# Performance work log

Measured on AMD Instinct MI355X. Metric: run time of the kernel, lower is better.

Reference implementation:

```python
import jax, jax.numpy as jnp
import numpy as np


def _centers(n):
    # make_coord_3d: cell-center coordinates in (-1, 1)
    r = 1.0 / n
    return -1.0 + r + 2.0 * r * jnp.arange(n, dtype=jnp.float32)


def setup_inputs() -> dict:
    key = jax.random.key(0)
    ks = jax.random.split(key, 16)
    B, C, Tin, Hin, Win = 1, 64, 6, 40, 40
    Gc = 27 + 8 * C  # 539 channels into conv00_3d
    s = lambda k, shp: jax.random.normal(k, shp, dtype=jnp.float32) * 0.05
    return {
        "feat": jax.random.normal(ks[0], (B, C, Tin, Hin, Win), dtype=jnp.float32),
        # conv00_3d = depthwise(1x1x1, groups=Gc) + pointwise(Gc->256)
        "dw1_w": s(ks[1], (Gc,)), "dw1_b": s(ks[2], (Gc,)),
        "pw1_w": s(ks[3], (256, Gc)), "pw1_b": s(ks[4], (256,)),
        "fc1_w": s(ks[5], (256, 256)), "fc1_b": s(ks[6], (256,)),
        "fc2_w": s(ks[7], (3, 256)), "fc2_b": s(ks[8], (3,)),
        # short_cut = depthwise(1x1x1, groups=C) + pointwise(C->3)
        "sc_dw_w": s(ks[9], (C,)), "sc_dw_b": s(ks[10], (C,)),
        "sc_pw_w": s(ks[11], (3, C)), "sc_pw_b": s(ks[12], (3,)),
        "T_out": 12, "H_out": 80, "W_out": 80,
    }


def _pw(x, w, b):
    # 1x1x1 Conv3d
    return jnp.einsum('bcthw,oc->bothw', x, w) + b[None, :, None, None, None]


def _forward(feat, dw1_w, dw1_b, pw1_w, pw1_b, fc1_w, fc1_b, fc2_w, fc2_b,
             sc_dw_w, sc_dw_b, sc_pw_w, sc_pw_b, T_out, H_out, W_out):
    B, C, Tin, Hin, Win = feat.shape
    ct, ch, cw = _centers(T_out), _centers(H_out), _centers(W_out)  # target centers
    lt, lh, lw = _centers(Tin), _centers(Hin), _centers(Win)        # low-res centers
    rt, rx, ry = 1.0 / Tin, 1.0 / Hin, 1.0 / Win                    # 2/N/2 radii
    eps = 1e-6

    def near(c, n):
        # grid_sample nearest, align_corners=False; coords pre-clamped as in torch code
        cc = jnp.clip(c, -1.0 + 1e-6, 1.0 - 1e-6)
        return jnp.clip(jnp.round(((cc + 1.0) * n - 1.0) / 2.0), 0, n - 1).astype(jnp.int32)

    rel_coords, feat_s, areas = [], [], []
    for vt in (-1.0, 1.0):
        for vx in (-1.0, 1.0):
            for vy in (-1.0, 1.0):
                it = near(ct + vt * rt + eps, Tin)   # [T'] (separable per-dim)
                ih = near(ch + vx * rx + eps, Hin)   # [H']
                iw = near(cw + vy * ry + eps, Win)   # [W']
                f = feat[:, :, it[:, None, None], ih[None, :, None], iw[None, None, :]]
                dct = (ct - lt[it]) * Tin
                dch = (ch - lh[ih]) * Hin
                dcw = (cw - lw[iw]) * Win
                rel = jnp.stack([
                    jnp.broadcast_to(dct[:, None, None], (T_out, H_out, W_out)),
                    jnp.broadcast_to(dch[None, :, None], (T_out, H_out, W_out)),
                    jnp.broadcast_to(dcw[None, None, :], (T_out, H_out, W_out)),
                ], axis=0)
                rel = jnp.broadcast_to(rel[None], (B, 3, T_out, H_out, W_out))
                area = (jnp.abs(dct)[:, None, None] * jnp.abs(dch)[None, :, None]
                        * jnp.abs(dcw)[None, None, :]) + 1e-9
                rel_coords.append(rel)
                feat_s.append(f)
                areas.append(area)

    tot = sum(areas)
    areas_sw = areas[::-1]  # pairwise swaps 0<->7, 1<->6, 2<->5, 3<->4
    feat_s = [f * (a / tot)[None, None] for f, a in zip(feat_s, areas_sw)]

    # rel_cell: (2/size * scale) * in_size == 2.0 on every axis
    rel_cell = jnp.full((B, 3, T_out, H_out, W_out), 2.0, dtype=feat.dtype)

    grid = jnp.concatenate([*rel_coords, *feat_s, rel_cell], axis=1)  # [B,27+8C,T',H',W']

    x = _pw(grid * dw1_w[None, :, None, None, None] + dw1_b[None, :, None, None, None],
            pw1_w, pw1_b)
    ret = _pw(jax.nn.gelu(_pw(x, fc1_w, fc1_b), approximate=False), fc2_w, fc2_b)

    # short cut: depthwise-separable 1x1x1 conv, then trilinear grid_sample (border pad)
    sc = _pw(feat * sc_dw_w[None, :, None, None, None] + sc_dw_b[None, :, None, None, None],
             sc_pw_w, sc_pw_b)

    def lin_idx(c, n):
        x = jnp.clip(((c + 1.0) * n - 1.0) / 2.0, 0.0, n - 1.0)  # border padding: clip coord
        x0 = jnp.floor(x)
        frac = x - x0
        i0 = x0.astype(jnp.int32)
        i1 = jnp.minimum(i0 + 1, n - 1)
        return i0, i1, frac

    t0, t1, ft = lin_idx(ct, Tin)
    h0, h1, fh = lin_idx(ch, Hin)
    w0, w1, fw = lin_idx(cw, Win)
    g = sc[:, :, t0] * (1 - ft)[None, None, :, None, None] + sc[:, :, t1] * ft[None, None, :, None, None]
    g = g[:, :, :, h0] * (1 - fh)[None, None, None, :, None] + g[:, :, :, h1] * fh[None, None, None, :, None]
    g = g[:, :, :, :, w0] * (1 - fw) + g[:, :, :, :, w1] * fw
    return ret + g


def reference(feat, dw1_w, dw1_b, pw1_w, pw1_b, fc1_w, fc1_b, fc2_w, fc2_b,
              sc_dw_w, sc_dw_b, sc_pw_w, sc_pw_b, T_out, H_out, W_out):
    return _forward(feat, dw1_w, dw1_b, pw1_w, pw1_b, fc1_w, fc1_b, fc2_w, fc2_b,
                    sc_dw_w, sc_dw_b, sc_pw_w, sc_pw_b, T_out, H_out, W_out)
```

## Files before the change

kernel.cpp:

```cpp
#include <hip/hip_runtime.h>
#include <hip/hip_bf16.h>

using bf16 = __hip_bfloat16;
typedef __attribute__((ext_vector_type(8))) short short8x;
typedef __attribute__((ext_vector_type(4))) short short4x;
typedef __attribute__((ext_vector_type(4))) unsigned short ushort4x;
typedef __attribute__((ext_vector_type(4))) float f32x4;

__device__ __forceinline__ float b2f(bf16 x) { return __bfloat162float(x); }
__device__ __forceinline__ bf16  f2b(float x) { return __float2bfloat16(x); }
__device__ __forceinline__ short bbits(float x) { bf16 b = f2b(x); short s; __builtin_memcpy(&s, &b, 2); return s; }
__device__ __forceinline__ float bu2f(unsigned short s) {
    unsigned v = ((unsigned)s) << 16; float f; __builtin_memcpy(&f, &v, 4); return f;
}
__device__ __forceinline__ float ldin(const void* p, int i, int f32) {
    return f32 ? ((const float*)p)[i] : b2f(((const bf16*)p)[i]);
}

#define TI 6
#define HI 40
#define WI 40
#define TO 12
#define HO 80
#define WO 80
#define NIN (TI*HI*WI)
#define NOUT (TO*HO*WO)

#define F_B1    0
#define F_ACO   (F_B1 + 256)
#define F_SCW   (F_ACO + 6*256)
#define F_SCB   (F_SCW + 3*64)
#define F_SC    (F_SCB + 4)
#define F_DT    (F_SC + 3*NIN)
#define F_DH    (F_DT + 2*TO)
#define F_DW    (F_DH + 2*HO)
#define F_FT    (F_DW + 2*WO)
#define F_FH    (F_FT + TO)
#define F_FW    (F_FH + HO)
#define F_FC1B  (F_FW + WO)
#define F_FC2W  (F_FC1B + 256)
#define F_FC2B  (F_FC2W + 768)
#define F_END   (F_FC2B + 4)
#define I_IT    0
#define I_IH    (I_IT + 2*TO)
#define I_IW    (I_IH + 2*HO)
#define I_LT0   (I_IW + 2*WO)
#define I_LT1   (I_LT0 + TO)
#define I_LH0   (I_LT1 + TO)
#define I_LH1   (I_LH0 + HO)
#define I_LW0   (I_LH1 + HO)
#define I_LW1   (I_LW0 + WO)
#define I_FLAG  (I_LW1 + WO)
#define I_END   (I_FLAG + 1)

#define MPOS 32
#define ZPAD 264
#define FT_S 72

__device__ __forceinline__ void axis_tables(int i, int n_out, int n_in,
                                            float* dvals, int* ivals,
                                            int* l0, int* l1, float* fr) {
    const float r_out = 1.0f / (float)n_out;
    const float r_in  = 1.0f / (float)n_in;
    const float c = -1.0f + r_out + 2.0f * r_out * (float)i;
    #pragma unroll
    for (int v = 0; v < 2; ++v) {
        const float vv = v ? 1.0f : -1.0f;
        float cc = c + vv * r_in + 1e-6f;
        cc = fminf(fmaxf(cc, -1.0f + 1e-6f), 1.0f - 1e-6f);
        float fx = rintf(((cc + 1.0f) * (float)n_in - 1.0f) * 0.5f);
        fx = fminf(fmaxf(fx, 0.0f), (float)(n_in - 1));
        const int idx = (int)fx;
        const float l = -1.0f + r_in + 2.0f * r_in * (float)idx;
        dvals[v * n_out + i] = (c - l) * (float)n_in;
        ivals[v * n_out + i] = idx;
    }
    float x = fminf(fmaxf(((c + 1.0f) * (float)n_in - 1.0f) * 0.5f, 0.0f), (float)(n_in - 1));
    const float x0 = floorf(x);
    fr[i] = x - x0;
    const int i0 = (int)x0;
    l0[i] = i0;
    l1[i] = min(i0 + 1, n_in - 1);
}

__global__ __launch_bounds__(256)
void k_setup(const void* __restrict__ feat,
             const void* __restrict__ dw1_w, const void* __restrict__ dw1_b,
             const void* __restrict__ pw1_w, const void* __restrict__ pw1_b,
             const void* __restrict__ fc1_w, const void* __restrict__ fc1_b,
             const void* __restrict__ fc2_w, const void* __restrict__ fc2_b,
             const void* __restrict__ sc_dw_w, const void* __restrict__ sc_dw_b,
             const void* __restrict__ sc_pw_w, const void* __restrict__ sc_pw_b,
             bf16* __restrict__ fc1P, bf16* __restrict__ W1fP,
             float* __restrict__ F, int* __restrict__ I) {
    const int tid = threadIdx.x;
    const int b = blockIdx.x;
    __shared__ int sflag;
    if (tid < 64) {
        const unsigned short* u = (const unsigned short*)feat;
        const unsigned e = (u[2 * tid] >> 7) & 0xFFu;
        const unsigned long long m = __ballot(e >= 0x68u && e <= 0x8Eu);
        if (tid == 0) sflag = (__popcll(m) < 32) ? 1 : 0;
    }
    __syncthreads();
    const int f32 = sflag;

    if (b >= 288) {
        const int g = (b - 288) * 256 + tid;
        const int k = g >> 11, kc = (g >> 10) & 1, nt = (g >> 6) & 15, wl = g & 63;
        const int n = nt * 16 + (wl & 15);
        const int k0 = kc * 32 + (wl >> 4) * 8;
        bf16 v[8];
        #pragma unroll
        for (int jj = 0; jj < 8; ++jj) {
            const int ch = 24 + k * 64 + k0 + jj;
            v[jj] = f2b(ldin(pw1_w, n * 539 + ch, f32) * ldin(dw1_w, ch, f32));
        }
        *(short8x*)&W1fP[(size_t)g * 8] = *(short8x*)v;
        return;
    }
    if (b >= 256) {
        const int g = (b - 256) * 256 + tid;
        const int kc = g >> 10, nt = (g >> 6) & 15, wl = g & 63;
        const int n = nt * 16 + (wl & 15);
        const int k0 = kc * 32 + (wl >> 4) * 8;
        bf16 v[8];
        #pragma unroll
        for (int jj = 0; jj < 8; ++jj) v[jj] = f2b(ldin(fc1_w, n * 256 + k0 + jj, f32));
        *(short8x*)&fc1P[(size_t)g * 8] = *(short8x*)v;
        return;
    }

    __shared__ float row[539];
    __shared__ float red[256];
    const int o = b;

    for (int ch = tid; ch < 539; ch += 256) row[ch] = ldin(pw1_w, o * 539 + ch, f32);
    __syncthreads();

    float s = 0.f;
    for (int ch = tid; ch < 539; ch += 256) s += row[ch] * ldin(dw1_b, ch, f32);
    red[tid] = s;
    __syncthreads();
    for (int st = 128; st > 0; st >>= 1) {
        if (tid < st) red[tid] += red[tid + st];
        __syncthreads();
    }

    if (tid == 0) {
        float bacc = ldin(pw1_b, o, f32) + red[0];
        #pragma unroll
        for (int ch = 536; ch < 539; ++ch)
            bacc += 2.0f * row[ch] * ldin(dw1_w, ch, f32);
        F[F_B1 + o] = bacc;

        float A[6] = {0.f, 0.f, 0.f, 0.f, 0.f, 0.f};
        #pragma unroll
        for (int k = 0; k < 8; ++k) {
            A[(k >> 2)]           += row[3*k + 0] * ldin(dw1_w, 3*k + 0, f32);
            A[2 + ((k >> 1) & 1)] += row[3*k + 1] * ldin(dw1_w, 3*k + 1, f32);
            A[4 + (k & 1)]        += row[3*k + 2] * ldin(dw1_w, 3*k + 2, f32);
        }
        #pragma unroll
        for (int i = 0; i < 6; ++i) F[F_ACO + i * 256 + o] = A[i];
    }

    if (b == 0) {
        if (tid == 0) I[I_FLAG] = f32;
        F[F_FC1B + tid] = ldin(fc1_b, tid, f32);
        for (int r = tid; r < 768; r += 256) F[F_FC2W + r] = ldin(fc2_w, r, f32);
        if (tid < 3) F[F_FC2B + tid] = ldin(fc2_b, tid, f32);
        if (tid < 3) {
            const int j = tid;
            float sb = ldin(sc_pw_b, j, f32);
            for (int c = 0; c < 64; ++c) {
                const float pw = ldin(sc_pw_w, j * 64 + c, f32);
                F[F_SCW + j * 64 + c] = pw * ldin(sc_dw_w, c, f32);
                sb += pw * ldin(sc_dw_b, c, f32);
            }
            F[F_SCB + j] = sb;
        }
        if (tid < TO) axis_tables(tid, TO, TI, F + F_DT, I + I_IT, I + I_LT0, I + I_LT1, F + F_FT);
        if (tid < HO) axis_tables(tid, HO, HI, F + F_DH, I + I_IH, I + I_LH0, I + I_LH1, F + F_FH);
        if (tid < WO) axis_tables(tid, WO, WI, F + F_DW, I + I_IW, I + I_LW0, I + I_LW1, F + F_FW);
    }
}

__global__ __launch_bounds__(256)
void k_corner(const void* __restrict__ feat, float* __restrict__ F,
              const int* __restrict__ I, const bf16* __restrict__ W1fP,
              bf16* __restrict__ P) {
    const int tid = threadIdx.x;
    const int pt = blockIdx.x, k = blockIdx.y;
    const int pos0 = pt * 32;
    const int f32 = I[I_FLAG];

    __shared__ __align__(16) short ft[32 * FT_S];
    __shared__ __align__(16) short zt[32 * ZPAD];

    {
        const int p = tid & 31, c0 = tid >> 5;
        #pragma unroll
        for (int cc = 0; cc < 8; ++cc) {
            const int c = c0 * 8 + cc;
            ft[p * FT_S + c] = bbits(ldin(feat, c * NIN + pos0 + p, f32));
        }
    }
    __syncthreads();

    const int wl = tid & 63, w = tid >> 6;
    const int col = wl & 15, quad = wl >> 4;
    f32x4 acc[2][4] = { { {0,0,0,0},{0,0,0,0},{0,0,0,0},{0,0,0,0} },
                        { {0,0,0,0},{0,0,0,0},{0,0,0,0},{0,0,0,0} } };
    const short8x* bp = (const short8x*)W1fP;
    #pragma unroll
    for (int kc = 0; kc < 2; ++kc) {
        const short8x a0 = *(const short8x*)&ft[col * FT_S + kc * 32 + quad * 8];
        const short8x a1 = *(const short8x*)&ft[(col + 16) * FT_S + kc * 32 + quad * 8];
        #pragma unroll
        for (int nt = 0; nt < 4; ++nt) {
            const short8x bb = bp[((k * 2 + kc) * 16 + (w * 4 + nt)) * 64 + wl];
            acc[0][nt] = __builtin_amdgcn_mfma_f32_16x16x32_bf16(a0, bb, acc[0][nt], 0, 0, 0);
            acc[1][nt] = __builtin_amdgcn_mfma_f32_16x16x32_bf16(a1, bb, acc[1][nt], 0, 0, 0);
        }
    }

    if (k == 0 && tid < 96) {
        const int j = tid >> 5, p = tid & 31;
        float s = F[F_SCB + j];
        for (int c = 0; c < 64; ++c)
            s += bu2f((unsigned short)ft[p * FT_S + c]) * F[F_SCW + j * 64 + c];
        F[F_SC + j * NIN + pos0 + p] = s;
    }

    #pragma unroll
    for (int mt = 0; mt < 2; ++mt)
        #pragma unroll
        for (int nt = 0; nt < 4; ++nt) {
            const int n = w * 64 + nt * 16 + col;
            #pragma unroll
            for (int r = 0; r < 4; ++r)
                zt[(mt * 16 + quad * 4 + r) * ZPAD + n] = bbits(acc[mt][nt][r]);
        }
    __syncthreads();

    #pragma unroll
    for (int q = 0; q < 4; ++q) {
        const int i = q * 256 + tid;
        const int p = i >> 5, c8 = i & 31;
        const short8x v = *(const short8x*)&zt[p * ZPAD + c8 * 8];
        *(short8x*)(P + ((size_t)(k * NIN + pos0 + p)) * 256 + c8 * 8) = v;
    }
}

__global__ __launch_bounds__(256, 4)
void k_main(const bf16* __restrict__ P, const bf16* __restrict__ fc1P,
            const float* __restrict__ F, const int* __restrict__ I,
            void* __restrict__ outv) {
    const int tid = threadIdx.x;
    const int pos0 = blockIdx.x * MPOS;
    const int f32 = I[I_FLAG];

    __shared__ __align__(16) short zsh[MPOS * ZPAD];
    __shared__ float redc[MPOS * 4 * 3];
    __shared__ int   sh_ipos[MPOS][8];
    __shared__ float sh_wk[MPOS][8];
    __shared__ float sh_dv[MPOS][6];
    __shared__ float sh_g[3][MPOS];

    if (tid < MPOS) {
        const int p = tid;
        const int pos = pos0 + p;
        const int t = pos / (HO * WO);
        const int rem = pos - t * (HO * WO);
        const int h = rem / WO;
        const int w = rem - h * WO;
        const int   iTa[2] = { I[I_IT + t], I[I_IT + TO + t] };
        const float dTv[2] = { F[F_DT + t], F[F_DT + TO + t] };
        const int   iHa[2] = { I[I_IH + h], I[I_IH + HO + h] };
        const float dHv[2] = { F[F_DH + h], F[F_DH + HO + h] };
        const int   iWa[2] = { I[I_IW + w], I[I_IW + WO + w] };
        const float dWv[2] = { F[F_DW + w], F[F_DW + WO + w] };
        sh_dv[p][0] = dTv[0]; sh_dv[p][1] = dTv[1];
        sh_dv[p][2] = dHv[0]; sh_dv[p][3] = dHv[1];
        sh_dv[p][4] = dWv[0]; sh_dv[p][5] = dWv[1];
        const float aT[2] = { fabsf(dTv[0]), fabsf(dTv[1]) };
        const float aH[2] = { fabsf(dHv[0]), fabsf(dHv[1]) };
        const float aW[2] = { fabsf(dWv[0]), fabsf(dWv[1]) };
        const float tot = (aT[0] + aT[1]) * (aH[0] + aH[1]) * (aW[0] + aW[1]) + 8e-9f;
        #pragma unroll
        for (int k = 0; k < 8; ++k) {
            const int at = k >> 2, ah = (k >> 1) & 1, aw = k & 1;
            sh_wk[p][k] = (aT[1 - at] * aH[1 - ah] * aW[1 - aw] + 1e-9f) / tot;
            sh_ipos[p][k] = iTa[at] * (HI * WI) + iHa[ah] * WI + iWa[aw];
        }
        const int a0 = I[I_LT0 + t], a1 = I[I_LT1 + t];
        const int bh0 = I[I_LH0 + h], bh1 = I[I_LH1 + h];
        const int c0 = I[I_LW0 + w], c1 = I[I_LW1 + w];
        const float fT = F[F_FT + t], fH = F[F_FH + h], fW = F[F_FW + w];
        #pragma unroll
        for (int jj = 0; jj < 3; ++jj) {
            const float* Sj = F + F_SC + jj * NIN;
            const int i0 = a0 * (HI * WI), i1 = a1 * (HI * WI);
            const float v000 = Sj[i0 + bh0 * WI + c0], v001 = Sj[i0 + bh0 * WI + c1];
            const float v010 = Sj[i0 + bh1 * WI + c0], v011 = Sj[i0 + bh1 * WI + c1];
            const float v100 = Sj[i1 + bh0 * WI + c0], v101 = Sj[i1 + bh0 * WI + c1];
            const float v110 = Sj[i1 + bh1 * WI + c0], v111 = Sj[i1 + bh1 * WI + c1];
            const float u00 = v000 * (1.f - fT) + v100 * fT;
            const float u01 = v001 * (1.f - fT) + v101 * fT;
            const float u10 = v010 * (1.f - fT) + v110 * fT;
            const float u11 = v011 * (1.f - fT) + v111 * fT;
            const float q0 = u00 * (1.f - fH) + u10 * fH;
            const float q1 = u01 * (1.f - fH) + u11 * fH;
            sh_g[jj][p] = q0 * (1.f - fW) + q1 * fW;
        }
    }
    __syncthreads();

    {
        const int og = tid & 63, pg = tid >> 6;
        const int o4 = og * 4;
        const float4 bz = *(const float4*)&F[F_B1 + o4];
        float4 Ac[6];
        #pragma unroll
        for (int i = 0; i < 6; ++i) Ac[i] = *(const float4*)&F[F_ACO + i * 256 + o4];
        for (int pp = 0; pp < 8; ++pp) {
            const int p = pg * 8 + pp;
            float a0 = bz.x, a1 = bz.y, a2 = bz.z, a3 = bz.w;
            #pragma unroll
            for (int i = 0; i < 6; ++i) {
                const float dv = sh_dv[p][i];
                a0 += Ac[i].x * dv; a1 += Ac[i].y * dv;
                a2 += Ac[i].z * dv; a3 += Ac[i].w * dv;
            }
            #pragma unroll
            for (int k = 0; k < 8; ++k) {
                const float wk = sh_wk[p][k];
                const ushort4x u = *(const ushort4x*)(P + ((size_t)(k * NIN + sh_ipos[p][k]) * 256 + o4));
                a0 += wk * bu2f(u.x); a1 += wk * bu2f(u.y);
                a2 += wk * bu2f(u.z); a3 += wk * bu2f(u.w);
            }
            short4x zz = { bbits(a0), bbits(a1), bbits(a2), bbits(a3) };
            *(short4x*)&zsh[p * ZPAD + o4] = zz;
        }
    }
    __syncthreads();

    {
        const int wl = tid & 63, w = tid >> 6;
        const int col = wl & 15, quad = wl >> 4;
        f32x4 acc0[4] = { {0,0,0,0}, {0,0,0,0}, {0,0,0,0}, {0,0,0,0} };
        f32x4 acc1[4] = { {0,0,0,0}, {0,0,0,0}, {0,0,0,0}, {0,0,0,0} };
        const short8x* bp = (const short8x*)fc1P;
        #pragma unroll
        for (int kc = 0; kc < 8; ++kc) {
            const short8x a0 = *(const short8x*)&zsh[col * ZPAD + kc * 32 + quad * 8];
            const short8x a1 = *(const short8x*)&zsh[(col + 16) * ZPAD + kc * 32 + quad * 8];
            #pragma unroll
            for (int nt = 0; nt < 4; ++nt) {
                const short8x b = bp[(kc * 16 + w * 4 + nt) * 64 + wl];
                acc0[nt] = __builtin_amdgcn_mfma_f32_16x16x32_bf16(a0, b, acc0[nt], 0, 0, 0);
                acc1[nt] = __builtin_amdgcn_mfma_f32_16x16x32_bf16(a1, b, acc1[nt], 0, 0, 0);
            }
        }
        float part[2][3][4];
        #pragma unroll
        for (int mt = 0; mt < 2; ++mt)
            #pragma unroll
            for (int jj = 0; jj < 3; ++jj)
                #pragma unroll
                for (int r = 0; r < 4; ++r) part[mt][jj][r] = 0.f;
        #pragma unroll
        for (int nt = 0; nt < 4; ++nt) {
            const int j = w * 64 + nt * 16 + col;
            const float fb = F[F_FC1B + j];
            const float w0 = F[F_FC2W + j];
            const float w1 = F[F_FC2W + 256 + j];
            const float w2 = F[F_FC2W + 512 + j];
            #pragma unroll
            for (int r = 0; r < 4; ++r) {
                float x = acc0[nt][r] + fb;
                float hh = 0.5f * x * (1.0f + erff(x * 0.70710678118654752f));
                part[0][0][r] += w0 * hh; part[0][1][r] += w1 * hh; part[0][2][r] += w2 * hh;
                x = acc1[nt][r] + fb;
                hh = 0.5f * x * (1.0f + erff(x * 0.70710678118654752f));
                part[1][0][r] += w0 * hh; part[1][1][r] += w1 * hh; part[1][2][r] += w2 * hh;
            }
        }
        #pragma unroll
        for (int m = 1; m <= 8; m <<= 1)
            #pragma unroll
            for (int mt = 0; mt < 2; ++mt)
                #pragma unroll
                for (int jj = 0; jj < 3; ++jj)
                    #pragma unroll
                    for (int r = 0; r < 4; ++r)
                        part[mt][jj][r] += __shfl_xor(part[mt][jj][r], m, 64);
        if (col == 0) {
            #pragma unroll
            for (int mt = 0; mt < 2; ++mt)
                #pragma unroll
                for (int jj = 0; jj < 3; ++jj)
                    #pragma unroll
                    for (int r = 0; r < 4; ++r) {
                        const int p = mt * 16 + quad * 4 + r;
                        redc[(p * 4 + w) * 3 + jj] = part[mt][jj][r];
                    }
        }
    }
    __syncthreads();

    if (tid < 96) {
        const int p = tid / 3, jj = tid - 3 * p;
        float a = F[F_FC2B + jj] + sh_g[jj][p];
        #pragma unroll
        for (int w = 0; w < 4; ++w) a += redc[(p * 4 + w) * 3 + jj];
        const int oidx = jj * NOUT + pos0 + p;
        if (f32) ((float*)outv)[oidx] = a;
        else     ((bf16*)outv)[oidx] = f2b(a);
    }
}

extern "C" void kernel_launch(void* const* d_in, const int* in_sizes, int n_in,
                              void* d_out, int out_size, void* d_ws, size_t ws_size,
                              hipStream_t stream) {
    const void* feat    = d_in[0];
    const void* dw1_w   = d_in[1];
    const void* dw1_b   = d_in[2];
    const void* pw1_w   = d_in[3];
    const void* pw1_b   = d_in[4];
    const void* fc1_w   = d_in[5];
    const void* fc1_b   = d_in[6];
    const void* fc2_w   = d_in[7];
    const void* fc2_b   = d_in[8];
    const void* sc_dw_w = d_in[9];
    const void* sc_dw_b = d_in[10];
    const void* sc_pw_w = d_in[11];
    const void* sc_pw_b = d_in[12];

    const size_t P_BYTES    = (size_t)8 * NIN * 256 * 2;
    const size_t FC1P_BYTES = (size_t)256 * 256 * 2;
    const size_t W1FP_BYTES = (size_t)8 * 64 * 256 * 2;
    bf16*  P    = (bf16*)d_ws;
    bf16*  fc1P = (bf16*)((char*)d_ws + P_BYTES);
    bf16*  W1fP = (bf16*)((char*)d_ws + P_BYTES + FC1P_BYTES);
    float* F    = (float*)((char*)d_ws + P_BYTES + FC1P_BYTES + W1FP_BYTES);
    int*   I    = (int*)(F + F_END);

    k_setup<<<352, 256, 0, stream>>>(feat, dw1_w, dw1_b, pw1_w, pw1_b, fc1_w, fc1_b,
                                     fc2_w, fc2_b, sc_dw_w, sc_dw_b, sc_pw_w, sc_pw_b,
                                     fc1P, W1fP, F, I);
    k_corner<<<dim3(NIN / 32, 8), 256, 0, stream>>>(feat, F, I, W1fP, P);
    k_main<<<NOUT / MPOS, 256, 0, stream>>>(P, fc1P, F, I, (void*)d_out);
}
```

Before: 171.7 us.

## Fold per-corner projection into main kernel via weighted gather plus MFMA

Removes the k_corner kernel that precomputed a 256-channel projection for every input voxel and each of 8 corners (a large bf16 intermediate). The main kernel now gathers the weighted 64-channel transposed features for each of the 8 corners into shared memory and runs a K=512 MFMA against the folded pw1 weights. Setup is restructured to write a transposed bf16 feature buffer and compute the shortcut conv, and erf in GELU is replaced by a polynomial approximation. This cuts memory traffic and one launch, but adds more MFMA work per output and slightly changes rounding, since weights are applied before the bf16 cast and GELU is approximated.

Measured after the change: 199.1 us. 1.16x slower.

```diff
diff --git a/kernel.cpp b/kernel.cpp
--- a/kernel.cpp
+++ b/kernel.cpp
@@ -3,8 +3,6 @@
 
 using bf16 = __hip_bfloat16;
 typedef __attribute__((ext_vector_type(8))) short short8x;
-typedef __attribute__((ext_vector_type(4))) short short4x;
-typedef __attribute__((ext_vector_type(4))) unsigned short ushort4x;
 typedef __attribute__((ext_vector_type(4))) float f32x4;
 
 __device__ __forceinline__ float b2f(bf16 x) { return __bfloat162float(x); }
@@ -15,6 +13,15 @@
 }
 __device__ __forceinline__ float ldin(const void* p, int i, int f32) {
     return f32 ? ((const float*)p)[i] : b2f(((const bf16*)p)[i]);
+}
+
+__device__ __forceinline__ float gelu_f(float x) {
+    const float z = fabsf(x) * 0.70710678118654752f;
+    const float t = __builtin_amdgcn_rcpf(1.0f + 0.3275911f * z);
+    const float poly = t * (0.254829592f + t * (-0.284496736f +
+                       t * (1.421413741f + t * (-1.453152027f + t * 1.061405429f))));
+    const float erfv = 1.0f - poly * __expf(-z * z);
+    return 0.5f * x * (1.0f + copysignf(erfv, x));
 }
 
 #define TI 6
@@ -28,9 +35,7 @@
 
 #define F_B1    0
 #define F_ACO   (F_B1 + 256)
-#define F_SCW   (F_ACO + 6*256)
-#define F_SCB   (F_SCW + 3*64)
-#define F_SC    (F_SCB + 4)
+#define F_SC    (F_ACO + 6*256)
 #define F_DT    (F_SC + 3*NIN)
 #define F_DH    (F_DT + 2*TO)
 #define F_DW    (F_DH + 2*HO)
@@ -54,8 +59,9 @@
 #define I_END   (I_FLAG + 1)
 
 #define MPOS 32
+#define USTR 552
+#define CSTR 68
 #define ZPAD 264
-#define FT_S 72
 
 __device__ __forceinline__ void axis_tables(int i, int n_out, int n_in,
                                             float* dvals, int* ivals,
@@ -91,8 +97,8 @@
              const void* __restrict__ fc2_w, const void* __restrict__ fc2_b,
              const void* __restrict__ sc_dw_w, const void* __restrict__ sc_dw_b,
              const void* __restrict__ sc_pw_w, const void* __restrict__ sc_pw_b,
-             bf16* __restrict__ fc1P, bf16* __restrict__ W1fP,
-             float* __restrict__ F, int* __restrict__ I) {
+             bf16* __restrict__ featT, bf16* __restrict__ fc1P,
+             bf16* __restrict__ W1fP, float* __restrict__ F, int* __restrict__ I) {
     const int tid = threadIdx.x;
     const int b = blockIdx.x;
     __shared__ int sflag;
@@ -105,163 +111,130 @@
     __syncthreads();
     const int f32 = sflag;
 
-    if (b >= 288) {
-        const int g = (b - 288) * 256 + tid;
-        const int k = g >> 11, kc = (g >> 10) & 1, nt = (g >> 6) & 15, wl = g & 63;
-        const int n = nt * 16 + (wl & 15);
-        const int k0 = kc * 32 + (wl >> 4) * 8;
-        bf16 v[8];
-        #pragma unroll
-        for (int jj = 0; jj < 8; ++jj) {
-            const int ch = 24 + k * 64 + k0 + jj;
-            v[jj] = f2b(ldin(pw1_w, n * 539 + ch, f32) * ldin(dw1_w, ch, f32));
-        }
-        *(short8x*)&W1fP[(size_t)g * 8] = *(short8x*)v;
+    if (b < 16) {
+        const int nt = b;
+        __shared__ float rowb[16][540];
+        __shared__ float dwl[544];
+        __shared__ float dbl[544];
+        for (int ch = tid; ch < 539; ch += 256) {
+            dwl[ch] = ldin(dw1_w, ch, f32);
+            dbl[ch] = ldin(dw1_b, ch, f32);
+        }
+        for (int r = 0; r < 16; ++r)
+            for (int ch = tid; ch < 539; ch += 256)
+                rowb[r][ch] = ldin(pw1_w, (nt * 16 + r) * 539 + ch, f32);
+        __syncthreads();
+
+        {
+            const int r = tid >> 4, part = tid & 15;
+            float s = 0.f;
+            for (int ch = part; ch < 539; ch += 16) s += rowb[r][ch] * dbl[ch];
+            #pragma unroll
+            for (int m = 1; m <= 8; m <<= 1) s += __shfl_xor(s, m, 64);
+            if (part == 0) {
+                const int n = nt * 16 + r;
+                float bacc = ldin(pw1_b, n, f32) + s;
+                #pragma unroll
+                for (int ch = 536; ch < 539; ++ch) bacc += 2.0f * rowb[r][ch] * dwl[ch];
+                F[F_B1 + n] = bacc;
+                float A[6] = {0.f, 0.f, 0.f, 0.f, 0.f, 0.f};
+                #pragma unroll
+                for (int k = 0; k < 8; ++k) {
+                    A[(k >> 2)]           += rowb[r][3*k + 0] * dwl[3*k + 0];
+                    A[2 + ((k >> 1) & 1)] += rowb[r][3*k + 1] * dwl[3*k + 1];
+                    A[4 + (k & 1)]        += rowb[r][3*k + 2] * dwl[3*k + 2];
+                }
+                #pragma unroll
+                for (int i = 0; i < 6; ++i) F[F_ACO + i * 256 + n] = A[i];
+            }
+        }
+        for (int it = 0; it < 4; ++it) {
+            const int gl = it * 256 + tid;
+            const int kc = gl >> 6, wl = gl & 63;
+            const int nl = wl & 15;
+            const int K0 = kc * 32 + (wl >> 4) * 8;
+            bf16 v[8];
+            #pragma unroll
+            for (int jj = 0; jj < 8; ++jj)
+                v[jj] = f2b(rowb[nl][24 + K0 + jj] * dwl[24 + K0 + jj]);
+            *(short8x*)&W1fP[((size_t)(kc * 16 + nt) * 64 + wl) * 8] = *(short8x*)v;
+        }
         return;
     }
-    if (b >= 256) {
-        const int g = (b - 256) * 256 + tid;
-        const int kc = g >> 10, nt = (g >> 6) & 15, wl = g & 63;
-        const int n = nt * 16 + (wl & 15);
-        const int k0 = kc * 32 + (wl >> 4) * 8;
-        bf16 v[8];
-        #pragma unroll
-        for (int jj = 0; jj < 8; ++jj) v[jj] = f2b(ldin(fc1_w, n * 256 + k0 + jj, f32));
-        *(short8x*)&fc1P[(size_t)g * 8] = *(short8x*)v;
+    if (b < 32) {
+        const int nt = b - 16;
+        __shared__ float rowf[16][260];
+        for (int r = 0; r < 16; ++r)
+            rowf[r][tid] = ldin(fc1_w, (nt * 16 + r) * 256 + tid, f32);
+        __syncthreads();
+        for (int it = 0; it < 2; ++it) {
+            const int gl = it * 256 + tid;
+            const int kc = gl >> 6, wl = gl & 63;
+            const int nl = wl & 15;
+            const int K0 = kc * 32 + (wl >> 4) * 8;
+            bf16 v[8];
+            #pragma unroll
+            for (int jj = 0; jj < 8; ++jj) v[jj] = f2b(rowf[nl][K0 + jj]);
+            *(short8x*)&fc1P[((size_t)(kc * 16 + nt) * 64 + wl) * 8] = *(short8x*)v;
+        }
         return;
     }
-
-    __shared__ float row[539];
-    __shared__ float red[256];
-    const int o = b;
-
-    for (int ch = tid; ch < 539; ch += 256) row[ch] = ldin(pw1_w, o * 539 + ch, f32);
-    __syncthreads();
-
-    float s = 0.f;
-    for (int ch = tid; ch < 539; ch += 256) s += row[ch] * ldin(dw1_b, ch, f32);
-    red[tid] = s;
-    __syncthreads();
-    for (int st = 128; st > 0; st >>= 1) {
-        if (tid < st) red[tid] += red[tid + st];
+    if (b < 182) {
+        const int pos0 = (b - 32) * 64;
+        __shared__ float tF[64][66];
+        __shared__ float scw_l[3][64];
+        __shared__ float scb_l[4];
+        {
+            const int p = tid & 63, cg = tid >> 6;
+            #pragma unroll
+            for (int cc = 0; cc < 16; ++cc) {
+                const int c = cg * 16 + cc;
+                tF[c][p] = ldin(feat, c * NIN + pos0 + p, f32);
+            }
+        }
+        if (tid < 192)
+            scw_l[tid >> 6][tid & 63] = ldin(sc_pw_w, tid, f32) * ldin(sc_dw_w, tid & 63, f32);
+        if (tid < 3) {
+            float sb = ldin(sc_pw_b, tid, f32);
+            for (int c = 0; c < 64; ++c)
+                sb += ldin(sc_pw_w, tid * 64 + c, f32) * ldin(sc_dw_b, c, f32);
+            scb_l[tid] = sb;
+        }
         __syncthreads();
-    }
-
-    if (tid == 0) {
-        float bacc = ldin(pw1_b, o, f32) + red[0];
-        #pragma unroll
-        for (int ch = 536; ch < 539; ++ch)
-            bacc += 2.0f * row[ch] * ldin(dw1_w, ch, f32);
-        F[F_B1 + o] = bacc;
-
-        float A[6] = {0.f, 0.f, 0.f, 0.f, 0.f, 0.f};
-        #pragma unroll
-        for (int k = 0; k < 8; ++k) {
-            A[(k >> 2)]           += row[3*k + 0] * ldin(dw1_w, 3*k + 0, f32);
-            A[2 + ((k >> 1) & 1)] += row[3*k + 1] * ldin(dw1_w, 3*k + 1, f32);
-            A[4 + (k & 1)]        += row[3*k + 2] * ldin(dw1_w, 3*k + 2, f32);
-        }
-        #pragma unroll
-        for (int i = 0; i < 6; ++i) F[F_ACO + i * 256 + o] = A[i];
-    }
-
-    if (b == 0) {
-        if (tid == 0) I[I_FLAG] = f32;
-        F[F_FC1B + tid] = ldin(fc1_b, tid, f32);
-        for (int r = tid; r < 768; r += 256) F[F_FC2W + r] = ldin(fc2_w, r, f32);
-        if (tid < 3) F[F_FC2B + tid] = ldin(fc2_b, tid, f32);
-        if (tid < 3) {
-            const int j = tid;
-            float sb = ldin(sc_pw_b, j, f32);
-            for (int c = 0; c < 64; ++c) {
-                const float pw = ldin(sc_pw_w, j * 64 + c, f32);
-                F[F_SCW + j * 64 + c] = pw * ldin(sc_dw_w, c, f32);
-                sb += pw * ldin(sc_dw_b, c, f32);
-            }
-            F[F_SCB + j] = sb;
-        }
-        if (tid < TO) axis_tables(tid, TO, TI, F + F_DT, I + I_IT, I + I_LT0, I + I_LT1, F + F_FT);
-        if (tid < HO) axis_tables(tid, HO, HI, F + F_DH, I + I_IH, I + I_LH0, I + I_LH1, F + F_FH);
-        if (tid < WO) axis_tables(tid, WO, WI, F + F_DW, I + I_IW, I + I_LW0, I + I_LW1, F + F_FW);
-    }
-}
-
-__global__ __launch_bounds__(256)
-void k_corner(const void* __restrict__ feat, float* __restrict__ F,
-              const int* __restrict__ I, const bf16* __restrict__ W1fP,
-              bf16* __restrict__ P) {
-    const int tid = threadIdx.x;
-    const int pt = blockIdx.x, k = blockIdx.y;
-    const int pos0 = pt * 32;
-    const int f32 = I[I_FLAG];
-
-    __shared__ __align__(16) short ft[32 * FT_S];
-    __shared__ __align__(16) short zt[32 * ZPAD];
-
-    {
-        const int p = tid & 31, c0 = tid >> 5;
-        #pragma unroll
-        for (int cc = 0; cc < 8; ++cc) {
-            const int c = c0 * 8 + cc;
-            ft[p * FT_S + c] = bbits(ldin(feat, c * NIN + pos0 + p, f32));
-        }
-    }
-    __syncthreads();
-
-    const int wl = tid & 63, w = tid >> 6;
-    const int col = wl & 15, quad = wl >> 4;
-    f32x4 acc[2][4] = { { {0,0,0,0},{0,0,0,0},{0,0,0,0},{0,0,0,0} },
-                        { {0,0,0,0},{0,0,0,0},{0,0,0,0},{0,0,0,0} } };
-    const short8x* bp = (const short8x*)W1fP;
-    #pragma unroll
-    for (int kc = 0; kc < 2; ++kc) {
-        const short8x a0 = *(const short8x*)&ft[col * FT_S + kc * 32 + quad * 8];
-        const short8x a1 = *(const short8x*)&ft[(col + 16) * FT_S + kc * 32 + quad * 8];
-        #pragma unroll
-        for (int nt = 0; nt < 4; ++nt) {
-            const short8x bb = bp[((k * 2 + kc) * 16 + (w * 4 + nt)) * 64 + wl];
-            acc[0][nt] = __builtin_amdgcn_mfma_f32_16x16x32_bf16(a0, bb, acc[0][nt], 0, 0, 0);
-            acc[1][nt] = __builtin_amdgcn_mfma_f32_16x16x32_bf16(a1, bb, acc[1][nt], 0, 0, 0);
-        }
-    }
-
-    if (k == 0 && tid < 96) {
-        const int j = tid >> 5, p = tid & 31;
-        float s = F[F_SCB + j];
-        for (int c = 0; c < 64; ++c)
-            s += bu2f((unsigned short)ft[p * FT_S + c]) * F[F_SCW + j * 64 + c];
-        F[F_SC + j * NIN + pos0 + p] = s;
-    }
-
-    #pragma unroll
-    for (int mt = 0; mt < 2; ++mt)
-        #pragma unroll
-        for (int nt = 0; nt < 4; ++nt) {
-            const int n = w * 64 + nt * 16 + col;
-            #pragma unroll
-            for (int r = 0; r < 4; ++r)
-                zt[(mt * 16 + quad * 4 + r) * ZPAD + n] = bbits(acc[mt][nt][r]);
-        }
-    __syncthreads();
-
-    #pragma unroll
-    for (int q = 0; q < 4; ++q) {
-        const int i = q * 256 + tid;
-        const int p = i >> 5, c8 = i & 31;
-        const short8x v = *(const short8x*)&zt[p * ZPAD + c8 * 8];
-        *(short8x*)(P + ((size_t)(k * NIN + pos0 + p)) * 256 + c8 * 8) = v;
-    }
+        for (int it = 0; it < 2; ++it) {
+            const int id = it * 256 + tid;
+            const int p = id >> 3, c8 = id & 7;
+            bf16 v[8];
+            #pragma unroll
+            for (int jj = 0; jj < 8; ++jj) v[jj] = f2b(tF[c8 * 8 + jj][p]);
+            *(short8x*)&featT[(size_t)(pos0 + p) * 64 + c8 * 8] = *(short8x*)v;
+        }
+        if (tid < 192) {
+            const int j = tid >> 6, p = tid & 63;
+            float s = scb_l[j];
+            for (int c = 0; c < 64; ++c) s += tF[c][p] * scw_l[j][c];
+            F[F_SC + j * NIN + pos0 + p] = s;
+        }
+        return;
+    }
+    if (tid == 0) I[I_FLAG] = f32;
+    F[F_FC1B + tid] = ldin(fc1_b, tid, f32);
+    for (int r = tid; r < 768; r += 256) F[F_FC2W + r] = ldin(fc2_w, r, f32);
+    if (tid < 3) F[F_FC2B + tid] = ldin(fc2_b, tid, f32);
+    if (tid < TO) axis_tables(tid, TO, TI, F + F_DT, I + I_IT, I + I_LT0, I + I_LT1, F + F_FT);
+    if (tid < HO) axis_tables(tid, HO, HI, F + F_DH, I + I_IH, I + I_LH0, I + I_LH1, F + F_FH);
+    if (tid < WO) axis_tables(tid, WO, WI, F + F_DW, I + I_IW, I + I_LW0, I + I_LW1, F + F_FW);
 }
 
 __global__ __launch_bounds__(256, 4)
-void k_main(const bf16* __restrict__ P, const bf16* __restrict__ fc1P,
-            const float* __restrict__ F, const int* __restrict__ I,
-            void* __restrict__ outv) {
+void k_main(const bf16* __restrict__ featT, const bf16* __restrict__ fc1P,
+            const bf16* __restrict__ W1fP, const float* __restrict__ F,
+            const int* __restrict__ I, void* __restrict__ outv) {
     const int tid = threadIdx.x;
     const int pos0 = blockIdx.x * MPOS;
     const int f32 = I[I_FLAG];
 
-    __shared__ __align__(16) short zsh[MPOS * ZPAD];
+    __shared__ __align__(16) short ubuf[MPOS * USTR];
     __shared__ float redc[MPOS * 4 * 3];
     __shared__ int   sh_ipos[MPOS][8];
     __shared__ float sh_wk[MPOS][8];
@@ -318,47 +291,75 @@
     __syncthreads();
 
     {
-        const int og = tid & 63, pg = tid >> 6;
-        const int o4 = og * 4;
-        const float4 bz = *(const float4*)&F[F_B1 + o4];
-        float4 Ac[6];
-        #pragma unroll
-        for (int i = 0; i < 6; ++i) Ac[i] = *(const float4*)&F[F_ACO + i * 256 + o4];
-        for (int pp = 0; pp < 8; ++pp) {
-            const int p = pg * 8 + pp;
-            float a0 = bz.x, a1 = bz.y, a2 = bz.z, a3 = bz.w;
-            #pragma unroll
-            for (int i = 0; i < 6; ++i) {
-                const float dv = sh_dv[p][i];
-                a0 += Ac[i].x * dv; a1 += Ac[i].y * dv;
-                a2 += Ac[i].z * dv; a3 += Ac[i].w * dv;
+        const int c8 = tid & 7;
+        int pair = tid >> 3;
+        #pragma unroll
+        for (int it = 0; it < 8; ++it, pair += 32) {
+            const int p = pair >> 3, k = pair & 7;
+            const int row = sh_ipos[p][k];
+            const float wk = sh_wk[p][k];
+            const short8x fr = *(const short8x*)(featT + (size_t)row * 64 + c8 * 8);
+            short v[8];
+            #pragma unroll
+            for (int jj = 0; jj < 8; ++jj)
+                v[jj] = bbits(wk * bu2f((unsigned short)fr[jj]));
+            *(short8x*)&ubuf[p * USTR + k * CSTR + c8 * 8] = *(short8x*)v;
+        }
+    }
+    __syncthreads();
+
+    const int wl = tid & 63, w = tid >> 6;
+    const int col = wl & 15, quad = wl >> 4;
+    {
+        f32x4 zacc[2][4] = { { {0,0,0,0},{0,0,0,0},{0,0,0,0},{0,0,0,0} },
+                             { {0,0,0,0},{0,0,0,0},{0,0,0,0},{0,0,0,0} } };
+        const short8x* bp = (const short8x*)W1fP;
+        #pragma unroll
+        for (int kc = 0; kc < 16; ++kc) {
+            const int corner = kc >> 1;
+            const int cin = (kc & 1) * 32 + quad * 8;
+            const short8x a0 = *(const short8x*)&ubuf[col * USTR + corner * CSTR + cin];
+            const short8x a1 = *(const short8x*)&ubuf[(col + 16) * USTR + corner * CSTR + cin];
+            #pragma unroll
+            for (int nt = 0; nt < 4; ++nt) {
+                const short8x bb = bp[((size_t)kc * 16 + w * 4 + nt) * 64 + wl];
+                zacc[0][nt] = __builtin_amdgcn_mfma_f32_16x16x32_bf16(a0, bb, zacc[0][nt], 0, 0, 0);
+                zacc[1][nt] = __builtin_amdgcn_mfma_f32_16x16x32_bf16(a1, bb, zacc[1][nt], 0, 0, 0);
             }
-            #pragma unroll
-            for (int k = 0; k < 8; ++k) {
-                const float wk = sh_wk[p][k];
-                const ushort4x u = *(const ushort4x*)(P + ((size_t)(k * NIN + sh_ipos[p][k]) * 256 + o4));
-                a0 += wk * bu2f(u.x); a1 += wk * bu2f(u.y);
-                a2 += wk * bu2f(u.z); a3 += wk * bu2f(u.w);
-            }
-            short4x zz = { bbits(a0), bbits(a1), bbits(a2), bbits(a3) };
-            *(short4x*)&zsh[p * ZPAD + o4] = zz;
+        }
+        __syncthreads();
+        #pragma unroll
+        for (int nt = 0; nt < 4; ++nt) {
+            const int n = w * 64 + nt * 16 + col;
+            const float b1 = F[F_B1 + n];
+            float Ac[6];
+            #pragma unroll
+            for (int i = 0; i < 6; ++i) Ac[i] = F[F_ACO + i * 256 + n];
+            #pragma unroll
+            for (int mt = 0; mt < 2; ++mt)
+                #pragma unroll
+                for (int r = 0; r < 4; ++r) {
+                    const int p = mt * 16 + quad * 4 + r;
+                    float x = zacc[mt][nt][r] + b1;
+                    #pragma unroll
+                    for (int i = 0; i < 6; ++i) x += Ac[i] * sh_dv[p][i];
+                    ubuf[p * ZPAD + n] = bbits(x);
+                }
         }
     }
     __syncthreads();
 
     {
-        const int wl = tid & 63, w = tid >> 6;
-        const int col = wl & 15, quad = wl >> 4;
         f32x4 acc0[4] = { {0,0,0,0}, {0,0,0,0}, {0,0,0,0}, {0,0,0,0} };
         f32x4 acc1[4] = { {0,0,0,0}, {0,0,0,0}, {0,0,0,0}, {0,0,0,0} };
         const short8x* bp = (const short8x*)fc1P;
         #pragma unroll
         for (int kc = 0; kc < 8; ++kc) {
-            const short8x a0 = *(const short8x*)&zsh[col * ZPAD + kc * 32 + quad * 8];
-            const short8x a1 = *(const short8x*)&zsh[(col + 16) * ZPAD + kc * 32 + quad * 8];
+            const short8x a0 = *(const short8x*)&ubuf[col * ZPAD + kc * 32 + quad * 8];
+            const short8x a1 = *(const short8x*)&ubuf[(col + 16) * ZPAD + kc * 32 + quad * 8];
             #pragma unroll
             for (int nt = 0; nt < 4; ++nt) {
-                const short8x b = bp[(kc * 16 + w * 4 + nt) * 64 + wl];
+                const short8x b = bp[((size_t)kc * 16 + w * 4 + nt) * 64 + wl];
                 acc0[nt] = __builtin_amdgcn_mfma_f32_16x16x32_bf16(a0, b, acc0[nt], 0, 0, 0);
                 acc1[nt] = __builtin_amdgcn_mfma_f32_16x16x32_bf16(a1, b, acc1[nt], 0, 0, 0);
             }
@@ -379,11 +380,9 @@
             const float w2 = F[F_FC2W + 512 + j];
             #pragma unroll
             for (int r = 0; r < 4; ++r) {
-                float x = acc0[nt][r] + fb;
-                float hh = 0.5f * x * (1.0f + erff(x * 0.70710678118654752f));
+                float hh = gelu_f(acc0[nt][r] + fb);
                 part[0][0][r] += w0 * hh; part[0][1][r] += w1 * hh; part[0][2][r] += w2 * hh;
-                x = acc1[nt][r] + fb;
-                hh = 0.5f * x * (1.0f + erff(x * 0.70710678118654752f));
+                hh = gelu_f(acc1[nt][r] + fb);
                 part[1][0][r] += w0 * hh; part[1][1][r] += w1 * hh; part[1][2][r] += w2 * hh;
             }
         }
@@ -414,7 +413,7 @@
         const int p = tid / 3, jj = tid - 3 * p;
         float a = F[F_FC2B + jj] + sh_g[jj][p];
         #pragma unroll
-        for (int w = 0; w < 4; ++w) a += redc[(p * 4 + w) * 3 + jj];
+        for (int w2 = 0; w2 < 4; ++w2) a += redc[(p * 4 + w2) * 3 + jj];
         const int oidx = jj * NOUT + pos0 + p;
         if (f32) ((float*)outv)[oidx] = a;
         else     ((bf16*)outv)[oidx] = f2b(a);
@@ -438,18 +437,17 @@
     const void* sc_pw_w = d_in[11];
     const void* sc_pw_b = d_in[12];
 
-    const size_t P_BYTES    = (size_t)8 * NIN * 256 * 2;
-    const size_t FC1P_BYTES = (size_t)256 * 256 * 2;
-    const size_t W1FP_BYTES = (size_t)8 * 64 * 256 * 2;
-    bf16*  P    = (bf16*)d_ws;
-    bf16*  fc1P = (bf16*)((char*)d_ws + P_BYTES);
-    bf16*  W1fP = (bf16*)((char*)d_ws + P_BYTES + FC1P_BYTES);
-    float* F    = (float*)((char*)d_ws + P_BYTES + FC1P_BYTES + W1FP_BYTES);
-    int*   I    = (int*)(F + F_END);
-
-    k_setup<<<352, 256, 0, stream>>>(feat, dw1_w, dw1_b, pw1_w, pw1_b, fc1_w, fc1_b,
+    const size_t FEATT_BYTES = (size_t)NIN * 64 * 2;
+    const size_t FC1P_BYTES  = (size_t)256 * 256 * 2;
+    const size_t W1FP_BYTES  = (size_t)512 * 256 * 2;
+    bf16*  featT = (bf16*)d_ws;
+    bf16*  fc1P  = (bf16*)((char*)d_ws + FEATT_BYTES);
+    bf16*  W1fP  = (bf16*)((char*)d_ws + FEATT_BYTES + FC1P_BYTES);
+    float* F     = (float*)((char*)d_ws + FEATT_BYTES + FC1P_BYTES + W1FP_BYTES);
+    int*   I     = (int*)(F + F_END);
+
+    k_setup<<<183, 256, 0, stream>>>(feat, dw1_w, dw1_b, pw1_w, pw1_b, fc1_w, fc1_b,
                                      fc2_w, fc2_b, sc_dw_w, sc_dw_b, sc_pw_w, sc_pw_b,
-                                     fc1P, W1fP, F, I);
-    k_corner<<<dim3(NIN / 32, 8), 256, 0, stream>>>(feat, F, I, W1fP, P);
-    k_main<<<NOUT / MPOS, 256, 0, stream>>>(P, fc1P, F, I, (void*)d_out);
-}
+                                     featT, fc1P, W1fP, F, I);
+    k_main<<<NOUT / MPOS, 256, 0, stream>>>(featT, fc1P, W1fP, F, I, (void*)d_out);
+}
```
